# Kernel tuning notes

Hardware: AMD Instinct MI355X
Metric: run time of the kernel (lower is better)

The kernel has to match this reference:

```python
import jax, jax.numpy as jnp
import numpy as np

# ---- fixed acquisition / imaging constants (from init_kwargs) ----
C = 1540.0            # speed of sound (m/s)
FS = 20e6             # sampling rate (Hz)
DR = C / FS           # meters per sample (dr)
R0 = 0.0              # range offset (data_span[0]=0)
TIK = 0.1             # tikhonov regularization
DB_MIN = -60.0
XPX, ZPX = 200, 200
N_ELEM, N_ENC, N_SAMP = 64, 32, 2048
PITCH = 0.3e-3


def setup_inputs() -> dict:
    key = jax.random.key(0)
    k1, k2, k3, k4 = jax.random.split(key, 4)
    datas = jax.random.normal(k1, (2, N_ELEM, N_SAMP, N_ELEM), dtype=jnp.float32)
    locs = jax.random.normal(k2, (2, 8, 3), dtype=jnp.float32)
    delays = 3.0 * jax.random.normal(k3, (N_ENC, N_ELEM), dtype=jnp.float32)   # samples
    weights = jax.random.normal(k4, (N_ENC, N_ELEM), dtype=jnp.float32)
    # calc_delays_beamforming: one-way path length (m) from each element to each pixel
    xe = (np.arange(N_ELEM) - (N_ELEM - 1) / 2.0) * PITCH            # element x (m)
    x = np.linspace(-15.0, 15.0, XPX) / 1000.0                        # pixel x (m)
    z = np.linspace(10.0, 40.0, ZPX) / 1000.0                         # pixel z (m)
    Z, X = np.meshgrid(z, x, indexing='ij')                           # [ZPX, XPX]
    d = np.sqrt((X[None] - xe[:, None, None]) ** 2 + Z[None] ** 2)    # [E, ZPX, XPX]
    bf_delays = jnp.asarray(d.reshape(N_ELEM, -1), dtype=jnp.float32) # [E, P]
    return {"datas": datas, "locs": locs, "delays": delays,
            "weights": weights, "bf_delays": bf_delays}


def _hilbert(x, axis):
    n = x.shape[axis]
    h = np.zeros(n, dtype=np.float32)
    h[0] = 1.0
    h[n // 2] = 1.0
    h[1:n // 2] = 2.0
    shape = [1] * x.ndim
    shape[axis] = n
    return jnp.fft.ifft(jnp.fft.fft(x, axis=axis) * jnp.asarray(h).reshape(shape), axis=axis)


def reference(datas, locs, delays, weights, bf_delays):
    B, T, S, R = datas.shape
    # ---- calc_H: frequency-domain encoding matrix H[f, tx, enc] ----
    f = jnp.fft.fftfreq(S).astype(jnp.float32)                                 # cycles/sample
    phase = jnp.exp(-2j * jnp.pi * f[:, None, None] * delays.T[None, :, :])    # [S, T, E]
    H = weights.T[None, :, :].astype(jnp.complex64) * phase                    # [S, T, E]
    # ---- calc_Hinv_tikhonov: per-freq (H^H H + lam I)^-1 H^H  -> [S, E, T] ----
    Hh = jnp.conj(H).transpose(0, 2, 1)                                        # [S, E, T]
    A = jnp.einsum('fet,ftd->fed', Hh, H) + TIK * jnp.eye(H.shape[2], dtype=jnp.complex64)
    Hinv = jnp.linalg.solve(A, Hh)                                             # [S, E, T]
    # ---- encode / decode (freq-domain matmuls, batched over B) ----
    F = jnp.fft.fft(datas, axis=2)                                             # [B, T, S, R]
    rf_enc = jnp.real(jnp.fft.ifft(jnp.einsum('fte,btfr->befr', H, F), axis=2))  # [B, E, S, R]
    F2 = jnp.fft.fft(rf_enc, axis=2)
    rf_dec = jnp.real(jnp.fft.ifft(jnp.einsum('fet,befr->btfr', Hinv, F2), axis=2))  # [B, T, S, R]
    iq = _hilbert(rf_dec, axis=2)                                              # analytic signal
    # ---- BeamformAD: delay-and-sum with linear interpolation ----
    d_rx = bf_delays                                                           # [R, P]
    P = d_rx.shape[1]

    def beamform_one(iq_b):                                                    # iq_b [T, S, R]
        iq_rs = iq_b.transpose(0, 2, 1)                                        # [T, R, S]
        def step(acc, xs):
            iq_t, d_t = xs                                                     # [R, S], [P]
            t = (d_t[None, :] + d_rx - R0) / DR                                # [R, P] fractional sample
            i0 = jnp.floor(t)
            frac = (t - i0)
            i0i = i0.astype(jnp.int32)
            valid = (i0i >= 0) & (i0i < S - 1)
            i0c = jnp.clip(i0i, 0, S - 2)
            v0 = jnp.take_along_axis(iq_t, i0c, axis=1)
            v1 = jnp.take_along_axis(iq_t, i0c + 1, axis=1)
            val = jnp.where(valid, v0 * (1.0 - frac) + v1 * frac, 0.0)
            return acc + val.sum(0), None
        acc0 = jnp.zeros((P,), dtype=iq_b.dtype)
        img, _ = jax.lax.scan(step, acc0, (iq_rs, d_rx))
        return img

    img = jax.vmap(beamform_one)(iq)                                           # [B, P]
    pred = jnp.abs(img).reshape(B, ZPX, XPX) + 1e-15
    mx = jnp.max(pred, axis=(1, 2), keepdims=True)
    out = jnp.clip(20.0 * jnp.log10(pred / mx), DB_MIN, 0.0)
    return out
```

## Files before the change

kernel.cpp:

```cpp
#include <hip/hip_runtime.h>
#include <math.h>

#define S_LEN 2048
#define K_HALF 1025
#define N_T 64
#define N_E 32
#define N_R 64
#define N_P 40000
#define XPX 200
#define ZPX 200
#define WIN0 256
#define WIN_LEN 1024
#define W_LDS 96
#define RSTRIDE 100
#define TWO_PI 6.283185307179586f
#define PITCH 0.3e-3f
#define PXSTEP (30.0f/199.0f*1e-3f)

#define FSZ   ((size_t)K_HALF * N_T * N_R)
#define YSZ   ((size_t)(N_T*N_R) * K_HALF)
#define DSZ   ((size_t)N_T * S_LEN * N_R)
#define IMGSZ ((size_t)8 * N_P)

__device__ __forceinline__ float2 cmul(float2 a, float2 b) {
  return make_float2(a.x*b.x - a.y*b.y, a.x*b.y + a.y*b.x);
}

__global__ void k_fft_fwd(const float* __restrict__ datas, float2* __restrict__ Fb) {
  __shared__ float2 xs0[S_LEN];
  __shared__ float2 xs1[S_LEN];
  __shared__ float2 tw[S_LEN/2];
  int t  = blockIdx.x;
  int rq = blockIdx.y;
  const float* db = datas + (size_t)blockIdx.z * DSZ;
  float2* F = Fb + (size_t)blockIdx.z * FSZ;
  int tid = threadIdx.x;
  for (int j = tid; j < S_LEN/2; j += 256) {
    float ang = -TWO_PI * (float)j / (float)S_LEN;
    tw[j] = make_float2(__cosf(ang), __sinf(ang));
  }
  int r0 = rq * 4;
  const float4* src = (const float4*)(db + (size_t)t * S_LEN * N_R + r0);
  for (int n = tid; n < S_LEN; n += 256) {
    int rn = __brev((unsigned)n) >> 21;
    float4 v = src[(size_t)n * (N_R/4)];
    xs0[rn] = make_float2(v.x, v.y);
    xs1[rn] = make_float2(v.z, v.w);
  }
  __syncthreads();
  for (int h = 1; h <= 256; h <<= 2) {
    int tsA = 1024 / h, tsB = 512 / h;
    for (int idx = tid; idx < 512; idx += 256) {
      int j = idx & (h - 1);
      int i0 = ((idx & ~(h - 1)) << 2) | j;
      float2 wA = tw[j * tsA];
      float2 wB = tw[j * tsB];
      {
        float2 a = xs0[i0], b = xs0[i0 + h], c = xs0[i0 + 2*h], d = xs0[i0 + 3*h];
        float2 tb = cmul(wA, b), td = cmul(wA, d);
        float2 u0 = make_float2(a.x+tb.x, a.y+tb.y);
        float2 u1 = make_float2(a.x-tb.x, a.y-tb.y);
        float2 u2 = make_float2(c.x+td.x, c.y+td.y);
        float2 u3 = make_float2(c.x-td.x, c.y-td.y);
        float2 v2 = cmul(wB, u2);
        float2 v3t = cmul(wB, u3);
        float2 v3 = make_float2(v3t.y, -v3t.x);
        xs0[i0]       = make_float2(u0.x+v2.x, u0.y+v2.y);
        xs0[i0 + 2*h] = make_float2(u0.x-v2.x, u0.y-v2.y);
        xs0[i0 + h]   = make_float2(u1.x+v3.x, u1.y+v3.y);
        xs0[i0 + 3*h] = make_float2(u1.x-v3.x, u1.y-v3.y);
      }
      {
        float2 a = xs1[i0], b = xs1[i0 + h], c = xs1[i0 + 2*h], d = xs1[i0 + 3*h];
        float2 tb = cmul(wA, b), td = cmul(wA, d);
        float2 u0 = make_float2(a.x+tb.x, a.y+tb.y);
        float2 u1 = make_float2(a.x-tb.x, a.y-tb.y);
        float2 u2 = make_float2(c.x+td.x, c.y+td.y);
        float2 u3 = make_float2(c.x-td.x, c.y-td.y);
        float2 v2 = cmul(wB, u2);
        float2 v3t = cmul(wB, u3);
        float2 v3 = make_float2(v3t.y, -v3t.x);
        xs1[i0]       = make_float2(u0.x+v2.x, u0.y+v2.y);
        xs1[i0 + 2*h] = make_float2(u0.x-v2.x, u0.y-v2.y);
        xs1[i0 + h]   = make_float2(u1.x+v3.x, u1.y+v3.y);
        xs1[i0 + 3*h] = make_float2(u1.x-v3.x, u1.y-v3.y);
      }
    }
    __syncthreads();
  }
  for (int idx = tid; idx < 1024; idx += 256) {
    float2 w = tw[idx];
    {
      float2 a = xs0[idx], b = xs0[idx + 1024];
      float2 tt = cmul(w, b);
      xs0[idx]        = make_float2(a.x+tt.x, a.y+tt.y);
      xs0[idx + 1024] = make_float2(a.x-tt.x, a.y-tt.y);
    }
    {
      float2 a = xs1[idx], b = xs1[idx + 1024];
      float2 tt = cmul(w, b);
      xs1[idx]        = make_float2(a.x+tt.x, a.y+tt.y);
      xs1[idx + 1024] = make_float2(a.x-tt.x, a.y-tt.y);
    }
  }
  __syncthreads();
  float2* Fp = F + (size_t)t * N_R + r0;
  for (int k = tid; k < K_HALF; k += 256) {
    int m = (S_LEN - k) & (S_LEN - 1);
    float2* dst = Fp + (size_t)k * (N_T*N_R);
    {
      float2 s = xs0[k], sm = xs0[m];
      *reinterpret_cast<float4*>(dst) =
        make_float4(0.5f*(s.x + sm.x), 0.5f*(s.y - sm.y),
                    0.5f*(s.y + sm.y), 0.5f*(sm.x - s.x));
    }
    {
      float2 s = xs1[k], sm = xs1[m];
      *reinterpret_cast<float4*>(dst + 2) =
        make_float4(0.5f*(s.x + sm.x), 0.5f*(s.y - sm.y),
                    0.5f*(s.y + sm.y), 0.5f*(sm.x - s.x));
    }
  }
}

__global__ __launch_bounds__(256) void k_solveM(const float* __restrict__ delays,
                                                const float* __restrict__ weights,
                                                float2* __restrict__ Hinv,
                                                float2* __restrict__ Hg) {
  __shared__ float2 Hs[N_T][N_E+1];
  __shared__ float2 AX[N_E][97];
  __shared__ float2 g[N_E];
  __shared__ float2 invds[N_E];
  int k = blockIdx.x;
  int tid = threadIdx.x;
  float fk = (float)k / (float)S_LEN;
  for (int i = tid; i < N_T*N_E; i += 256) {
    int t = i & 63, e = i >> 6;
    float d = delays[e*N_T + t], w = weights[e*N_T + t];
    float ang = -TWO_PI * fk * d;
    Hs[t][e] = make_float2(w*__cosf(ang), w*__sinf(ang));
  }
  __syncthreads();
  {
    float2* Hp = Hg + (size_t)k * (N_T*N_E);
    for (int i = tid; i < N_T*N_E; i += 256) {
      int t = i >> 5, e = i & 31;
      Hp[i] = Hs[t][e];
    }
  }
  for (int s = tid; s < 528; s += 256) {
    int dd = (int)((sqrtf(8.f*(float)s + 1.f) - 1.f) * 0.5f);
    while (dd*(dd+1)/2 > s) --dd;
    while ((dd+1)*(dd+2)/2 <= s) ++dd;
    int e = s - dd*(dd+1)/2;
    float ar = 0.f, ai = 0.f;
    for (int tt = 0; tt < N_T; ++tt) {
      float2 he = Hs[tt][e], hd = Hs[tt][dd];
      ar += he.x*hd.x + he.y*hd.y;
      ai += he.x*hd.y - he.y*hd.x;
    }
    if (e == dd) ar += 0.1f;
    AX[e][dd] = make_float2(ar, ai);
  }
  __syncthreads();
  for (int idx = tid; idx < N_E*N_E; idx += 256) {
    int e = idx >> 5, dd = idx & 31;
    if (e > dd) {
      float2 u = AX[dd][e];
      AX[e][dd] = make_float2(u.x, -u.y);
    }
  }
  for (int idx = tid; idx < N_E*N_T; idx += 256) {
    int e = idx >> 6, t = idx & 63;
    float2 h = Hs[t][e];
    AX[e][32 + t] = make_float2(h.x, -h.y);
  }
  __syncthreads();
  int j = tid >> 3;
  int cb = tid & 7;
  for (int i = 0; i < N_E; ++i) {
    if (tid < N_E) {
      float2 dg = AX[i][i];
      float rden = 1.f / (dg.x*dg.x + dg.y*dg.y);
      float2 iv = make_float2(dg.x*rden, -dg.y*rden);
      g[tid] = cmul(AX[tid][i], iv);
      if (tid == 0) invds[i] = iv;
    }
    __syncthreads();
    if (j != i) {
      float2 gj = g[j];
      int cbase = cb * 12;
      #pragma unroll
      for (int u = 0; u < 12; ++u) {
        int c = cbase + u;
        float2 piv = AX[i][c];
        float2 v = AX[j][c];
        AX[j][c] = make_float2(v.x - (gj.x*piv.x - gj.y*piv.y),
                               v.y - (gj.x*piv.y + gj.y*piv.x));
      }
    }
    __syncthreads();
  }
  bool edge = (k == 0) || (k == S_LEN/2);
  float coef = edge ? (1.0f/(float)S_LEN) : (2.0f/(float)S_LEN);
  float2* Op = Hinv + (size_t)k * (N_E*N_T);
  for (int idx = tid; idx < N_E*N_T; idx += 256) {
    int e = idx >> 6, t = idx & 63;
    float2 v = cmul(AX[e][32+t], invds[e]);
    Op[idx] = make_float2(v.x*coef, v.y*coef);
  }
}

__global__ __launch_bounds__(256) void k_combine2(const float2* __restrict__ Fb,
                                                  const float2* __restrict__ Hinv,
                                                  const float2* __restrict__ Hg,
                                                  float2* __restrict__ Ykb) {
  __shared__ float2 Fs[N_T][N_R];
  int wg = blockIdx.x;
  int xcd = wg & 7, ci = wg >> 3;
  int k = (xcd == 0) ? ci : (129 + (xcd - 1) * 128 + ci);
  const float2* F = Fb + (size_t)blockIdx.z * FSZ;
  float2* Yk = Ykb + (size_t)blockIdx.z * YSZ;
  int tid = threadIdx.x;
  {
    const float4* Fk = (const float4*)(F + (size_t)k * (N_T*N_R));
    float4* FsL = (float4*)Fs;
    for (int i = tid; i < N_T*N_R/2; i += 256)
      FsL[i] = Fk[i];
  }
  __syncthreads();
  bool edge = (k == 0) || (k == S_LEN/2);
  int lane = tid & 63;
  int w = __builtin_amdgcn_readfirstlane(tid >> 6);
  const float2* Hrow = Hg + (size_t)k * (N_T*N_E) + w*8;
  float2 ga[8];
  #pragma unroll
  for (int i = 0; i < 8; ++i) ga[i] = make_float2(0.f, 0.f);
  for (int t = 0; t < N_T; ++t) {
    float2 f = Fs[t][lane];
    #pragma unroll
    for (int i = 0; i < 8; ++i) {
      float2 h = Hrow[t*N_E + i];
      ga[i].x += h.x*f.x - h.y*f.y;
      ga[i].y += h.x*f.y + h.y*f.x;
    }
  }
  __syncthreads();
  if (edge) {
    #pragma unroll
    for (int i = 0; i < 8; ++i) ga[i].y = 0.f;
  }
  float2* Gs = &Fs[0][0];
  #pragma unroll
  for (int i = 0; i < 8; ++i)
    Gs[(w*8 + i)*N_R + lane] = ga[i];
  __syncthreads();
  const float2* Hk = Hinv + (size_t)k * (N_E*N_T) + w*16;
  float2 acc[16];
  #pragma unroll
  for (int i = 0; i < 16; ++i) acc[i] = make_float2(0.f, 0.f);
  for (int e = 0; e < N_E; ++e) {
    float2 f = Gs[e*N_R + lane];
    const float2* hrow = Hk + e*N_T;
    #pragma unroll
    for (int i = 0; i < 16; ++i) {
      float2 m = hrow[i];
      acc[i].x += m.x*f.x - m.y*f.y;
      acc[i].y += m.x*f.y + m.y*f.x;
    }
  }
  float2* Yp = Yk + (size_t)(w*16*N_R + lane) * K_HALF + k;
  #pragma unroll
  for (int i = 0; i < 16; ++i)
    Yp[(size_t)i * (N_R*K_HALF)] = make_float2(acc[i].x, edge ? 0.f : acc[i].y);
}

__global__ void k_ifft(const float2* __restrict__ Ykb, float2* __restrict__ iqb) {
  __shared__ float2 xsA[S_LEN];
  __shared__ float2 xsB[S_LEN];
  __shared__ float2 tw[S_LEN/2];
  int wg = blockIdx.x;
  int j0 = ((wg & 7) * 256 + (wg >> 3)) * 2;
  const float2* Yk = Ykb + (size_t)blockIdx.z * YSZ;
  float2* iq = iqb + (size_t)blockIdx.z * FSZ;
  int tid = threadIdx.x;
  for (int q = tid; q < S_LEN/2; q += 256) {
    float ang = TWO_PI * (float)q / (float)S_LEN;
    tw[q] = make_float2(__cosf(ang), __sinf(ang));
  }
  const float2* rowAg = Yk + (size_t)j0 * K_HALF;
  const float2* rowBg = rowAg + K_HALF;
  for (int n = tid; n < S_LEN; n += 256) {
    int rn = __brev((unsigned)n) >> 21;
    float2 a = make_float2(0.f, 0.f), b = make_float2(0.f, 0.f);
    if (n < K_HALF) { a = rowAg[n]; b = rowBg[n]; }
    xsA[rn] = a;
    xsB[rn] = b;
  }
  __syncthreads();
  for (int h = 1; h <= 256; h <<= 2) {
    int tsA = 1024 / h, tsB = 512 / h;
    for (int idx = tid; idx < 512; idx += 256) {
      int j = idx & (h - 1);
      int i0 = ((idx & ~(h - 1)) << 2) | j;
      float2 wA = tw[j * tsA];
      float2 wB = tw[j * tsB];
      {
        float2 a = xsA[i0], b = xsA[i0 + h], c = xsA[i0 + 2*h], d = xsA[i0 + 3*h];
        float2 tb = cmul(wA, b), td = cmul(wA, d);
        float2 u0 = make_float2(a.x+tb.x, a.y+tb.y);
        float2 u1 = make_float2(a.x-tb.x, a.y-tb.y);
        float2 u2 = make_float2(c.x+td.x, c.y+td.y);
        float2 u3 = make_float2(c.x-td.x, c.y-td.y);
        float2 v2 = cmul(wB, u2);
        float2 v3t = cmul(wB, u3);
        float2 v3 = make_float2(-v3t.y, v3t.x);
        xsA[i0]       = make_float2(u0.x+v2.x, u0.y+v2.y);
        xsA[i0 + 2*h] = make_float2(u0.x-v2.x, u0.y-v2.y);
        xsA[i0 + h]   = make_float2(u1.x+v3.x, u1.y+v3.y);
        xsA[i0 + 3*h] = make_float2(u1.x-v3.x, u1.y-v3.y);
      }
      {
        float2 a = xsB[i0], b = xsB[i0 + h], c = xsB[i0 + 2*h], d = xsB[i0 + 3*h];
        float2 tb = cmul(wA, b), td = cmul(wA, d);
        float2 u0 = make_float2(a.x+tb.x, a.y+tb.y);
        float2 u1 = make_float2(a.x-tb.x, a.y-tb.y);
        float2 u2 = make_float2(c.x+td.x, c.y+td.y);
        float2 u3 = make_float2(c.x-td.x, c.y-td.y);
        float2 v2 = cmul(wB, u2);
        float2 v3t = cmul(wB, u3);
        float2 v3 = make_float2(-v3t.y, v3t.x);
        xsB[i0]       = make_float2(u0.x+v2.x, u0.y+v2.y);
        xsB[i0 + 2*h] = make_float2(u0.x-v2.x, u0.y-v2.y);
        xsB[i0 + h]   = make_float2(u1.x+v3.x, u1.y+v3.y);
        xsB[i0 + 3*h] = make_float2(u1.x-v3.x, u1.y-v3.y);
      }
    }
    __syncthreads();
  }
  float2* rowA = iq + (size_t)j0 * WIN_LEN;
  float2* rowB = iq + (size_t)(j0+1) * WIN_LEN;
  for (int idx = tid; idx < 1024; idx += 256) {
    float2 w = tw[idx];
    {
      float2 a = xsA[idx], b = xsA[idx + 1024];
      float2 tt = cmul(w, b);
      if (idx >= WIN0) rowA[idx - WIN0] = make_float2(a.x+tt.x, a.y+tt.y);
      else             rowA[idx + (1024 - WIN0)] = make_float2(a.x-tt.x, a.y-tt.y);
    }
    {
      float2 a = xsB[idx], b = xsB[idx + 1024];
      float2 tt = cmul(w, b);
      if (idx >= WIN0) rowB[idx - WIN0] = make_float2(a.x+tt.x, a.y+tt.y);
      else             rowB[idx + (1024 - WIN0)] = make_float2(a.x-tt.x, a.y-tt.y);
    }
  }
}

__global__ __launch_bounds__(256, 2) void k_beamform(const float2* __restrict__ iqb,
                                                     float2* __restrict__ imgpb) {
  __shared__ float winRe[N_R][RSTRIDE];
  __shared__ float winIm[N_R][RSTRIDE];
  __shared__ float basef[N_R];
  int wg = blockIdx.x;
  int tg = wg & 7;
  int bx = wg >> 3;
  const float2* iq = iqb + (size_t)blockIdx.z * FSZ;
  float2* imgp = imgpb + (size_t)blockIdx.z * IMGSZ;
  int tid = threadIdx.x;
  int tx = tid & 15, tz = tid >> 4;
  int x = (bx % 13) * 16 + tx;
  int z = (bx / 13) * 16 + tz;
  bool ok = (x < XPX) && (z < ZPX);
  int p = z * XPX + x;
  const float invDR = (float)(20.0e6 / 1540.0);
  float xm = fmaf((float)x, PXSTEP, -15e-3f);
  float zm = fmaf((float)z, PXSTEP, 10e-3f);
  float z2 = zm * zm;
  float xm0 = fmaf((float)((bx % 13) * 16), PXSTEP, -15e-3f);
  float xm1 = xm0 + 15.f * PXSTEP;
  float zb0 = fmaf((float)((bx / 13) * 16), PXSTEP, 10e-3f);
  float zb2 = zb0 * zb0;
  float di[64];
  #pragma unroll
  for (int e = 0; e < 64; ++e) {
    float xe = ((float)e - 31.5f) * PITCH;
    float dx = xm - xe;
    di[e] = sqrtf(fmaf(dx, dx, z2)) * invDR;
  }
  int rrow = tid >> 2, sub = tid & 3;
  float xer = ((float)rrow - 31.5f) * PITCH;
  float dxr = fminf(fmaxf(xer, xm0), xm1) - xer;
  float minDR_r = sqrtf(fmaf(dxr, dxr, zb2)) * invDR;
  float ar = 0.f, ai = 0.f;
  #pragma unroll 1
  for (int t8 = 0; t8 < 8; ++t8) {
    int t = tg * 8 + t8;
    float xet = ((float)t - 31.5f) * PITCH;
    float dxt = fminf(fmaxf(xet, xm0), xm1) - xet;
    float minDT = sqrtf(fmaf(dxt, dxt, zb2)) * invDR;
    int base = (int)floorf(minDT + minDR_r) - 1;
    base = min(base, WIN0 + WIN_LEN - W_LDS);
    if (sub == 0) basef[rrow] = (float)base;
    const float2* rowp = iq + ((size_t)t * N_R + rrow) * WIN_LEN + (base - WIN0);
    #pragma unroll
    for (int jj = 0; jj < 12; ++jj) {
      int s = sub * 24 + jj * 2;
      float4 v = *reinterpret_cast<const float4*>(rowp + s);
      winRe[rrow][s]   = v.x;  winRe[rrow][s+1] = v.z;
      winIm[rrow][s]   = v.y;  winIm[rrow][s+1] = v.w;
    }
    __syncthreads();
    float dxT = xm - xet;
    float dti = sqrtf(fmaf(dxT, dxT, z2)) * invDR;
    #pragma unroll
    for (int r = 0; r < 64; ++r) {
      float rel = dti + di[r] - basef[r];
      int o = (int)rel;
      float fr = rel - (float)o;
      float re0 = winRe[r][o], re1 = winRe[r][o+1];
      float im0 = winIm[r][o], im1 = winIm[r][o+1];
      ar += re0 + fr * (re1 - re0);
      ai += im0 + fr * (im1 - im0);
    }
    __syncthreads();
  }
  if (ok) imgp[(size_t)tg * N_P + p] = make_float2(ar, ai);
}

__global__ void k_magred(const float2* __restrict__ imgpb, float* __restrict__ mag) {
  int p = blockIdx.x*256 + threadIdx.x;
  if (p >= N_P) return;
  const float2* imgp = imgpb + (size_t)blockIdx.z * IMGSZ;
  float ar = 0.f, ai = 0.f;
  #pragma unroll
  for (int g = 0; g < 8; ++g) {
    float2 v = imgp[(size_t)g * N_P + p];
    ar += v.x; ai += v.y;
  }
  mag[(size_t)blockIdx.z * N_P + p] = sqrtf(ar*ar + ai*ai);
}

__global__ void k_max(const float* __restrict__ mag, float* __restrict__ mx) {
  __shared__ float red[256];
  int b = blockIdx.x, tid = threadIdx.x;
  float m = 0.f;
  for (int i = tid; i < N_P; i += 256) m = fmaxf(m, mag[(size_t)b*N_P + i]);
  red[tid] = m; __syncthreads();
  for (int s = 128; s > 0; s >>= 1) {
    if (tid < s) red[tid] = fmaxf(red[tid], red[tid+s]);
    __syncthreads();
  }
  if (tid == 0) mx[b] = red[0] + 1e-15f;
}

__global__ void k_final(const float* __restrict__ mag, const float* __restrict__ mx,
                        float* __restrict__ out) {
  int i = blockIdx.x*256 + threadIdx.x;
  if (i >= 2*N_P) return;
  int b = i / N_P;
  float v = (mag[i] + 1e-15f) / mx[b];
  float db = 20.f * log10f(v);
  out[i] = fminf(fmaxf(db, -60.f), 0.f);
}

extern "C" void kernel_launch(void* const* d_in, const int* in_sizes, int n_in,
                              void* d_out, int out_size, void* d_ws, size_t ws_size,
                              hipStream_t stream) {
  const float* datas   = (const float*)d_in[0];
  const float* delays  = (const float*)d_in[2];
  const float* weights = (const float*)d_in[3];
  float* out = (float*)d_out;
  char* ws = (char*)d_ws;

  const size_t HINV_B = (size_t)K_HALF*N_E*N_T*sizeof(float2);
  const size_t HG_B   = (size_t)K_HALF*N_T*N_E*sizeof(float2);
  const size_t F_B    = FSZ*sizeof(float2);
  const size_t Y_B    = YSZ*sizeof(float2);
  const size_t IMG_B  = IMGSZ*sizeof(float2);
  const size_t MAG_B  = (size_t)2*N_P*sizeof(float);
  const size_t DUAL_NEED = HINV_B + HG_B + 2*Y_B + 2*F_B + 2*IMG_B + MAG_B + 256;

  if (ws_size >= DUAL_NEED) {
    size_t off = 0;
    float2* Hinv = (float2*)(ws + off); off += HINV_B;
    float2* Hg   = (float2*)(ws + off); off += HG_B;
    float2* Yk2  = (float2*)(ws + off); off += 2*Y_B;
    float2* F2   = (float2*)(ws + off); off += 2*F_B;
    float2* iq2  = (float2*)F2;
    float2* imgp2= (float2*)(ws + off); off += 2*IMG_B;
    float*  mag  = (float*)(ws + off);  off += MAG_B;
    float*  mx   = (float*)(ws + off);

    k_solveM<<<dim3(K_HALF), dim3(256), 0, stream>>>(delays, weights, Hinv, Hg);
    k_fft_fwd<<<dim3(64, 16, 2), dim3(256), 0, stream>>>(datas, F2);
    k_combine2<<<dim3(K_HALF, 1, 2), dim3(256), 0, stream>>>(F2, Hinv, Hg, Yk2);
    k_ifft<<<dim3(N_T*N_R/2, 1, 2), dim3(256), 0, stream>>>(Yk2, iq2);
    k_beamform<<<dim3(1352, 1, 2), dim3(256), 0, stream>>>(iq2, imgp2);
    k_magred<<<dim3((N_P+255)/256, 1, 2), dim3(256), 0, stream>>>(imgp2, mag);
    k_max<<<dim3(2), dim3(256), 0, stream>>>(mag, mx);
    k_final<<<dim3((2*N_P+255)/256), dim3(256), 0, stream>>>(mag, mx, out);
  } else {
    size_t off = 0;
    float2* Hinv = (float2*)(ws + off); off += HINV_B;
    float2* Hg   = (float2*)(ws + off); off += HG_B;
    float2* Yk   = (float2*)(ws + off); off += Y_B;
    float2* F    = (float2*)(ws + off); off += F_B;
    float2* iq   = (float2*)F;
    float2* imgp = (float2*)(ws + off); off += IMG_B;
    float*  mag  = (float*)(ws + off);  off += MAG_B;
    float*  mx   = (float*)(ws + off);

    k_solveM<<<dim3(K_HALF), dim3(256), 0, stream>>>(delays, weights, Hinv, Hg);
    for (int b = 0; b < 2; ++b) {
      const float* db = datas + (size_t)b * DSZ;
      k_fft_fwd<<<dim3(64, 16, 1), dim3(256), 0, stream>>>(db, F);
      k_combine2<<<dim3(K_HALF, 1, 1), dim3(256), 0, stream>>>(F, Hinv, Hg, Yk);
      k_ifft<<<dim3(N_T*N_R/2, 1, 1), dim3(256), 0, stream>>>(Yk, iq);
      k_beamform<<<dim3(1352, 1, 1), dim3(256), 0, stream>>>(iq, imgp);
      k_magred<<<dim3((N_P+255)/256, 1, 1), dim3(256), 0, stream>>>(imgp, mag + (size_t)b*N_P);
    }
    k_max<<<dim3(2), dim3(256), 0, stream>>>(mag, mx);
    k_final<<<dim3((2*N_P+255)/256), dim3(256), 0, stream>>>(mag, mx, out);
  }
}
```

Baseline: 560.2 us.

## Restructure beamform tiles: 16x8 pixels, split receivers across thread pairs, quantized LDS delays

The beamform kernel moves from 16x16 pixel tiles, one thread per pixel, to 16x8 tiles with two threads per pixel, each summing half the receive elements and combining through a shuffle. The per-pixel 64-entry receive-delay register array is replaced by 16-bit fixed-point delays precomputed into LDS. The LDS window shrinks from 96 to 72 samples per row because the base offset is now based on floors. This is meant to cut register pressure and raise parallelism, at the cost of reloading windows for twice as many blocks, a small quantization error in delays, and a tighter window that could read out of bounds.

Result: slower. 715.2 us (+27.7%).

```diff
diff --git a/kernel.cpp b/kernel.cpp
--- a/kernel.cpp
+++ b/kernel.cpp
@@ -11,11 +11,13 @@
 #define ZPX 200
 #define WIN0 256
 #define WIN_LEN 1024
-#define W_LDS 96
-#define RSTRIDE 100
+#define W_LDS 72
+#define WSTR 75
+#define HOFF 2401
 #define TWO_PI 6.283185307179586f
 #define PITCH 0.3e-3f
 #define PXSTEP (30.0f/199.0f*1e-3f)
+#define INV_Q  (1.0f/1024.0f)
 
 #define FSZ   ((size_t)K_HALF * N_T * N_R)
 #define YSZ   ((size_t)(N_T*N_R) * K_HALF)
@@ -359,19 +361,20 @@
 
 __global__ __launch_bounds__(256, 2) void k_beamform(const float2* __restrict__ iqb,
                                                      float2* __restrict__ imgpb) {
-  __shared__ float winRe[N_R][RSTRIDE];
-  __shared__ float winIm[N_R][RSTRIDE];
-  __shared__ float basef[N_R];
+  __shared__ float winRe[2*HOFF];
+  __shared__ float winIm[2*HOFF];
+  __shared__ unsigned short q2[32*256];
+  __shared__ float cRs[N_R];
   int wg = blockIdx.x;
   int tg = wg & 7;
   int bx = wg >> 3;
   const float2* iq = iqb + (size_t)blockIdx.z * FSZ;
   float2* imgp = imgpb + (size_t)blockIdx.z * IMGSZ;
   int tid = threadIdx.x;
-  int tx = tid & 15, tz = tid >> 4;
-  int x = (bx % 13) * 16 + tx;
-  int z = (bx / 13) * 16 + tz;
-  bool ok = (x < XPX) && (z < ZPX);
+  int px = tid >> 1, rh = tid & 1;
+  int x = (bx % 13) * 16 + (px & 15);
+  int z = (bx / 13) * 8 + (px >> 4);
+  bool ok = (x < XPX);
   int p = z * XPX + x;
   const float invDR = (float)(20.0e6 / 1540.0);
   float xm = fmaf((float)x, PXSTEP, -15e-3f);
@@ -379,53 +382,67 @@
   float z2 = zm * zm;
   float xm0 = fmaf((float)((bx % 13) * 16), PXSTEP, -15e-3f);
   float xm1 = xm0 + 15.f * PXSTEP;
-  float zb0 = fmaf((float)((bx / 13) * 16), PXSTEP, 10e-3f);
+  float zb0 = fmaf((float)((bx / 13) * 8), PXSTEP, 10e-3f);
   float zb2 = zb0 * zb0;
-  float di[64];
-  #pragma unroll
-  for (int e = 0; e < 64; ++e) {
-    float xe = ((float)e - 31.5f) * PITCH;
-    float dx = xm - xe;
-    di[e] = sqrtf(fmaf(dx, dx, z2)) * invDR;
+  if (tid < N_R) {
+    float xe = ((float)tid - 31.5f) * PITCH;
+    float dxr = fminf(fmaxf(xe, xm0), xm1) - xe;
+    cRs[tid] = floorf(sqrtf(fmaf(dxr, dxr, zb2)) * invDR);
+  }
+  __syncthreads();
+  for (int v = tid; v < 64*128; v += 256) {
+    int r = v >> 7, pxx = v & 127;
+    float xp = fmaf((float)((bx % 13) * 16 + (pxx & 15)), PXSTEP, -15e-3f);
+    float zp = fmaf((float)((bx / 13) * 8 + (pxx >> 4)), PXSTEP, 10e-3f);
+    float xe = ((float)r - 31.5f) * PITCH;
+    float dx = xp - xe;
+    float di = sqrtf(fmaf(dx, dx, zp*zp)) * invDR - cRs[r];
+    q2[(r & 31) * 256 + pxx * 2 + (r >> 5)] = (unsigned short)(di * 1024.f + 0.5f);
   }
   int rrow = tid >> 2, sub = tid & 3;
-  float xer = ((float)rrow - 31.5f) * PITCH;
-  float dxr = fminf(fmaxf(xer, xm0), xm1) - xer;
-  float minDR_r = sqrtf(fmaf(dxr, dxr, zb2)) * invDR;
+  float cRrow = cRs[rrow];
+  int qbase = px * 2 + rh;
   float ar = 0.f, ai = 0.f;
+  __syncthreads();
   #pragma unroll 1
   for (int t8 = 0; t8 < 8; ++t8) {
     int t = tg * 8 + t8;
     float xet = ((float)t - 31.5f) * PITCH;
     float dxt = fminf(fmaxf(xet, xm0), xm1) - xet;
-    float minDT = sqrtf(fmaf(dxt, dxt, zb2)) * invDR;
-    int base = (int)floorf(minDT + minDR_r) - 1;
-    base = min(base, WIN0 + WIN_LEN - W_LDS);
-    if (sub == 0) basef[rrow] = (float)base;
-    const float2* rowp = iq + ((size_t)t * N_R + rrow) * WIN_LEN + (base - WIN0);
+    float cTf = floorf(sqrtf(fmaf(dxt, dxt, zb2)) * invDR);
+    {
+      int base = (int)cTf + (int)cRrow;
+      const float2* rowp = iq + ((size_t)t * N_R + rrow) * WIN_LEN + (base - WIN0);
+      int offR = (rrow >> 5) * HOFF + (rrow & 31) * WSTR;
+      #pragma unroll
+      for (int jj = 0; jj < 9; ++jj) {
+        int s = sub * 18 + jj * 2;
+        float4 v = *reinterpret_cast<const float4*>(rowp + s);
+        winRe[offR + s]     = v.x;  winRe[offR + s + 1] = v.z;
+        winIm[offR + s]     = v.y;  winIm[offR + s + 1] = v.w;
+      }
+    }
+    __syncthreads();
+    float dxT = xm - xet;
+    float relT = sqrtf(fmaf(dxT, dxT, z2)) * invDR - cTf;
+    int hbase = rh * HOFF;
     #pragma unroll
-    for (int jj = 0; jj < 12; ++jj) {
-      int s = sub * 24 + jj * 2;
-      float4 v = *reinterpret_cast<const float4*>(rowp + s);
-      winRe[rrow][s]   = v.x;  winRe[rrow][s+1] = v.z;
-      winIm[rrow][s]   = v.y;  winIm[rrow][s+1] = v.w;
-    }
-    __syncthreads();
-    float dxT = xm - xet;
-    float dti = sqrtf(fmaf(dxT, dxT, z2)) * invDR;
-    #pragma unroll
-    for (int r = 0; r < 64; ++r) {
-      float rel = dti + di[r] - basef[r];
+    for (int i = 0; i < 32; ++i) {
+      float qv = (float)q2[i * 256 + qbase] * INV_Q;
+      float rel = relT + qv;
       int o = (int)rel;
       float fr = rel - (float)o;
-      float re0 = winRe[r][o], re1 = winRe[r][o+1];
-      float im0 = winIm[r][o], im1 = winIm[r][o+1];
+      int woff = hbase + i * WSTR + o;
+      float re0 = winRe[woff], re1 = winRe[woff + 1];
+      float im0 = winIm[woff], im1 = winIm[woff + 1];
       ar += re0 + fr * (re1 - re0);
       ai += im0 + fr * (im1 - im0);
     }
     __syncthreads();
   }
-  if (ok) imgp[(size_t)tg * N_P + p] = make_float2(ar, ai);
+  ar += __shfl_xor(ar, 1);
+  ai += __shfl_xor(ai, 1);
+  if (rh == 0 && ok) imgp[(size_t)tg * N_P + p] = make_float2(ar, ai);
 }
 
 __global__ void k_magred(const float2* __restrict__ imgpb, float* __restrict__ mag) {
@@ -496,7 +513,7 @@
     k_fft_fwd<<<dim3(64, 16, 2), dim3(256), 0, stream>>>(datas, F2);
     k_combine2<<<dim3(K_HALF, 1, 2), dim3(256), 0, stream>>>(F2, Hinv, Hg, Yk2);
     k_ifft<<<dim3(N_T*N_R/2, 1, 2), dim3(256), 0, stream>>>(Yk2, iq2);
-    k_beamform<<<dim3(1352, 1, 2), dim3(256), 0, stream>>>(iq2, imgp2);
+    k_beamform<<<dim3(2600, 1, 2), dim3(256), 0, stream>>>(iq2, imgp2);
     k_magred<<<dim3((N_P+255)/256, 1, 2), dim3(256), 0, stream>>>(imgp2, mag);
     k_max<<<dim3(2), dim3(256), 0, stream>>>(mag, mx);
     k_final<<<dim3((2*N_P+255)/256), dim3(256), 0, stream>>>(mag, mx, out);
@@ -517,7 +534,7 @@
       k_fft_fwd<<<dim3(64, 16, 1), dim3(256), 0, stream>>>(db, F);
       k_combine2<<<dim3(K_HALF, 1, 1), dim3(256), 0, stream>>>(F, Hinv, Hg, Yk);
       k_ifft<<<dim3(N_T*N_R/2, 1, 1), dim3(256), 0, stream>>>(Yk, iq);
-      k_beamform<<<dim3(1352, 1, 1), dim3(256), 0, stream>>>(iq, imgp);
+      k_beamform<<<dim3(2600, 1, 1), dim3(256), 0, stream>>>(iq, imgp);
       k_magred<<<dim3((N_P+255)/256, 1, 1), dim3(256), 0, stream>>>(imgp, mag + (size_t)b*N_P);
     }
     k_max<<<dim3(2), dim3(256), 0, stream>>>(mag, mx);
```
